# Kernel tuning notes

Measured on AMD Instinct MI355X. Metric: run time of the kernel, lower is better.

The kernel has to match this reference:

```python
import jax, jax.numpy as jnp
import numpy as np

N_NODES = 50000
N_EDGES = 800000
IN_DIM = 256
HID = 128
OUT = 128
HEADS = 2
EDGE_DIM = 2
NEG_SLOPE = 0.2


def _add_self_loops(src, dst, edge_attr, n):
    # PyG add_self_loops with fill_value='mean': self-loop edge_attr is the
    # mean of edge_attr over edges entering each node (0 if no in-edges).
    sums = jax.ops.segment_sum(edge_attr, dst, num_segments=n)
    cnt = jax.ops.segment_sum(jnp.ones((edge_attr.shape[0],), edge_attr.dtype), dst, num_segments=n)
    loop_attr = sums / jnp.maximum(cnt, 1.0)[:, None]
    ar = jnp.arange(n, dtype=src.dtype)
    return (jnp.concatenate([src, ar]), jnp.concatenate([dst, ar]),
            jnp.concatenate([edge_attr, loop_attr], axis=0))


def _gat_conv(x, src, dst, edge_attr, W, att_src, att_dst, We, att_e, bias, H, C):
    n = x.shape[0]
    xh = (x @ W).reshape(n, H, C)                      # [N,H,C]
    a_src = jnp.sum(xh * att_src, axis=-1)             # [N,H]
    a_dst = jnp.sum(xh * att_dst, axis=-1)             # [N,H]
    eh = (edge_attr @ We).reshape(-1, H, C)            # [E,H,C]
    a_e = jnp.sum(eh * att_e, axis=-1)                 # [E,H]
    logits = jax.nn.leaky_relu(a_src[src] + a_dst[dst] + a_e, NEG_SLOPE)
    # segment softmax over destination node
    m = jax.ops.segment_max(logits, dst, num_segments=n)
    m = jnp.where(jnp.isfinite(m), m, 0.0)
    ex = jnp.exp(logits - m[dst])
    denom = jax.ops.segment_sum(ex, dst, num_segments=n)
    alpha = ex / (denom[dst] + 1e-16)                  # [E,H]
    msg = xh[src] * alpha[:, :, None]                  # [E,H,C]
    out = jax.ops.segment_sum(msg, dst, num_segments=n)  # [N,H,C]
    return out.reshape(n, H * C) + bias


def setup_inputs() -> dict:
    key = jax.random.key(0)
    ks = jax.random.split(key, 16)
    s = 0.05
    inp = {
        "x": jax.random.normal(ks[0], (N_NODES, IN_DIM), jnp.float32),
        "edge_index": jax.random.randint(ks[1], (2, N_EDGES), 0, N_NODES, jnp.int32),
        "edge_attr": jax.random.normal(ks[2], (N_EDGES, EDGE_DIM), jnp.float32),
        # conv1: heads=2
        "W1": jax.random.normal(ks[3], (IN_DIM, HEADS * HID), jnp.float32) * s,
        "att_src1": jax.random.normal(ks[4], (HEADS, HID), jnp.float32) * s,
        "att_dst1": jax.random.normal(ks[5], (HEADS, HID), jnp.float32) * s,
        "We1": jax.random.normal(ks[6], (EDGE_DIM, HEADS * HID), jnp.float32) * s,
        "att_e1": jax.random.normal(ks[7], (HEADS, HID), jnp.float32) * s,
        "b1": jnp.zeros((HEADS * HID,), jnp.float32),
        # conv2: heads=1
        "W2": jax.random.normal(ks[8], (HEADS * HID, OUT), jnp.float32) * s,
        "att_src2": jax.random.normal(ks[9], (1, OUT), jnp.float32) * s,
        "att_dst2": jax.random.normal(ks[10], (1, OUT), jnp.float32) * s,
        "We2": jax.random.normal(ks[11], (EDGE_DIM, OUT), jnp.float32) * s,
        "att_e2": jax.random.normal(ks[12], (1, OUT), jnp.float32) * s,
        "b2": jnp.zeros((OUT,), jnp.float32),
    }
    return inp


def reference(x, edge_index, edge_attr, W1, att_src1, att_dst1, We1, att_e1, b1,
              W2, att_src2, att_dst2, We2, att_e2, b2):
    src, dst = edge_index[0], edge_index[1]
    src, dst, ea = _add_self_loops(src, dst, edge_attr, x.shape[0])
    h = _gat_conv(x, src, dst, ea, W1, att_src1, att_dst1, We1, att_e1, b1, HEADS, HID)
    h = jax.nn.elu(h)
    out = _gat_conv(h, src, dst, ea, W2, att_src2, att_dst2, We2, att_e2, b2, 1, OUT)
    return out
```

## Files before the change

### kernel.cpp

```cpp
#include <hip/hip_runtime.h>
#include <math.h>

#define N_NODES 50000
#define N_EDGES 800000
#define EP (N_EDGES + N_NODES)
#define NEG_SLOPE 0.2f
#define SCAN_BLOCKS ((N_NODES + 255) / 256)

typedef __attribute__((ext_vector_type(8))) short bf16x8;
typedef __attribute__((ext_vector_type(4))) float f32x4;

__device__ __forceinline__ unsigned short f2bf(float f) {
  unsigned u = __float_as_uint(f);
  unsigned r = (u + 0x7FFFu + ((u >> 16) & 1u)) >> 16;
  return (unsigned short)r;
}
__device__ __forceinline__ float bf2f(unsigned short b) {
  return __uint_as_float(((unsigned)b) << 16);
}

__global__ void fill_u32(unsigned* p, unsigned v, int n) {
  int i = blockIdx.x * blockDim.x + threadIdx.x;
  if (i < n) p[i] = v;
}

__global__ void rank_pass(const int* __restrict__ ei, int* __restrict__ cnt,
                          int* __restrict__ rank) {
  int e = blockIdx.x * blockDim.x + threadIdx.x;
  if (e >= N_EDGES) return;
  rank[e] = atomicAdd(&cnt[ei[N_EDGES + e]], 1);
}

__global__ void block_sums(const int* __restrict__ cnt, int* __restrict__ bsum) {
  __shared__ int ws[4];
  int b = blockIdx.x;
  int i = b * 256 + threadIdx.x;
  int v = (i < N_NODES) ? (cnt[i] + 1) : 0;
  #pragma unroll
  for (int off = 32; off > 0; off >>= 1) v += __shfl_down(v, off);
  if ((threadIdx.x & 63) == 0) ws[threadIdx.x >> 6] = v;
  __syncthreads();
  if (threadIdx.x == 0) bsum[b] = ws[0] + ws[1] + ws[2] + ws[3];
}

__global__ void emit_rowptr(const int* __restrict__ cnt, const int* __restrict__ bsum,
                            int* __restrict__ rowptr) {
  __shared__ int buf[2][256];
  int b = blockIdx.x, t = threadIdx.x;
  int vb = (t < SCAN_BLOCKS) ? bsum[t] : 0;
  buf[0][t] = vb;
  __syncthreads();
  int cur = 0;
  for (int off = 1; off < 256; off <<= 1) {
    int x = buf[cur][t];
    if (t >= off) x += buf[cur][t - off];
    buf[cur ^ 1][t] = x;
    cur ^= 1;
    __syncthreads();
  }
  int base = buf[cur][b] - ((b < SCAN_BLOCKS) ? bsum[b] : 0);
  __syncthreads();
  int i = b * 256 + t;
  int v = (i < N_NODES) ? (cnt[i] + 1) : 0;
  buf[cur][t] = v;
  __syncthreads();
  int c2 = cur;
  for (int off = 1; off < 256; off <<= 1) {
    int x = buf[c2][t];
    if (t >= off) x += buf[c2][t - off];
    buf[c2 ^ 1][t] = x;
    c2 ^= 1;
    __syncthreads();
  }
  int incl = buf[c2][t];
  if (i < N_NODES) {
    rowptr[i] = base + incl - v;
    if (i == N_NODES - 1) rowptr[N_NODES] = base + incl;
  }
}

__global__ void scatter_pass(const int* __restrict__ ei, const float* __restrict__ ea,
                             const int* __restrict__ rowptr, const int* __restrict__ rank,
                             uint2* __restrict__ ecsr) {
  int e = blockIdx.x * blockDim.x + threadIdx.x;
  if (e >= N_EDGES) return;
  int d = ei[N_EDGES + e];
  int pos = rowptr[d] + rank[e];
  uint2 v;
  v.x = (unsigned)ei[e];
  v.y = (unsigned)f2bf(ea[2 * e]) | ((unsigned)f2bf(ea[2 * e + 1]) << 16);
  ecsr[pos] = v;
}

#define MISC_LATTR 196
#define MISC_BT    384
__global__ void prep_misc(const int* __restrict__ rowptr, uint2* __restrict__ ecsr,
                          const float* __restrict__ W1, const float* __restrict__ W2,
                          unsigned short* __restrict__ b1h, unsigned short* __restrict__ b1l,
                          unsigned short* __restrict__ b2h, unsigned short* __restrict__ b2l,
                          const float* __restrict__ ae1, const float* __restrict__ ae2,
                          const float* __restrict__ We1, const float* __restrict__ We2,
                          float* __restrict__ Ae) {
  int b = blockIdx.x;
  int t = threadIdx.x;
  if (b < MISC_LATTR) {
    int n = b * 256 + t;
    if (n >= N_NODES) return;
    int beg = rowptr[n], end = rowptr[n + 1];
    float s0 = 0.f, s1 = 0.f;
    for (int j = beg; j < end - 1; ++j) {
      unsigned p = ecsr[j].y;
      s0 += __uint_as_float(p << 16);
      s1 += __uint_as_float(p & 0xFFFF0000u);
    }
    float c = fmaxf((float)(end - 1 - beg), 1.0f);
    uint2 m;
    m.x = (unsigned)n;
    m.y = (unsigned)f2bf(s0 / c) | ((unsigned)f2bf(s1 / c) << 16);
    ecsr[end - 1] = m;
  } else if (b < MISC_LATTR + MISC_BT) {
    int nb = b - MISC_LATTR;
    float v; unsigned short* ph; unsigned short* pl; int idx;
    if (nb < 256) { v = W1[t * 256 + nb];         ph = b1h; pl = b1l; idx = nb * 256 + t; }
    else          { v = W2[t * 128 + (nb - 256)]; ph = b2h; pl = b2l; idx = (nb - 256) * 256 + t; }
    unsigned short h = f2bf(v);
    ph[idx] = h;
    pl[idx] = f2bf(v - bf2f(h));
  } else {
    if (t >= 64) return;
    int bb = b - (MISC_LATTR + MISC_BT);
    float s = 0.f;
    if (bb < 4) {
      int d = bb >> 1, h = bb & 1;
      for (int c = t; c < 128; c += 64)
        s += We1[d * 256 + h * 128 + c] * ae1[h * 128 + c];
    } else {
      int d = bb - 4;
      for (int c = t; c < 128; c += 64)
        s += We2[d * 128 + c] * ae2[c];
    }
    for (int off = 32; off > 0; off >>= 1) s += __shfl_down(s, off);
    if (t == 0) Ae[bb] = s;
  }
}

template <int H>
__global__ __launch_bounds__(256) void gemm_split(
    const float* __restrict__ A,
    const unsigned short* __restrict__ Bth, const unsigned short* __restrict__ Btl,
    unsigned short* __restrict__ C, int M, int N,
    const float* __restrict__ att_src, const float* __restrict__ att_dst,
    float* __restrict__ asrc, float* __restrict__ adst) {
  __shared__ __attribute__((aligned(16))) unsigned short As[2][64][40];
  __shared__ __attribute__((aligned(16))) unsigned short Bs[2][128][40];
  __shared__ float redS[2][64], redD[2][64];
  int bm = blockIdx.y * 64, bn = blockIdx.x * 128;
  int tid = threadIdx.x;
  int l = tid & 63;
  int wid = tid >> 6;
  int wr = wid >> 1, wc = wid & 1;
  int rr = l & 15, kc = l >> 4;

  f32x4 acc[2][4];
  #pragma unroll
  for (int i = 0; i < 2; ++i)
    #pragma unroll
    for (int j = 0; j < 4; ++j)
      acc[i][j] = (f32x4){0.f, 0.f, 0.f, 0.f};

  int ar = tid >> 2, ac = tid & 3;
  int gm = bm + ar;

  for (int kt = 0; kt < 8; ++kt) {
    int k0 = kt * 32;
    float4 f0 = {0.f, 0.f, 0.f, 0.f}, f1 = f0;
    if (gm < M) {
      f0 = *(const float4*)(A + (size_t)gm * 256 + k0 + ac * 8);
      f1 = *(const float4*)(A + (size_t)gm * 256 + k0 + ac * 8 + 4);
    }
    float f[8] = {f0.x, f0.y, f0.z, f0.w, f1.x, f1.y, f1.z, f1.w};
    unsigned hw[4], lw[4];
    #pragma unroll
    for (int q = 0; q < 4; ++q) {
      unsigned short ha = f2bf(f[2 * q]),  hb = f2bf(f[2 * q + 1]);
      unsigned short la = f2bf(f[2 * q] - bf2f(ha)), lb = f2bf(f[2 * q + 1] - bf2f(hb));
      hw[q] = (unsigned)ha | ((unsigned)hb << 16);
      lw[q] = (unsigned)la | ((unsigned)lb << 16);
    }
    *(uint4*)&As[0][ar][ac * 8] = make_uint4(hw[0], hw[1], hw[2], hw[3]);
    *(uint4*)&As[1][ar][ac * 8] = make_uint4(lw[0], lw[1], lw[2], lw[3]);
    #pragma unroll
    for (int p = 0; p < 2; ++p) {
      int id = tid + p * 256;
      int nn = id >> 2, cc = id & 3;
      *(uint4*)&Bs[0][nn][cc * 8] = *(const uint4*)(Bth + (size_t)(bn + nn) * 256 + k0 + cc * 8);
      *(uint4*)&Bs[1][nn][cc * 8] = *(const uint4*)(Btl + (size_t)(bn + nn) * 256 + k0 + cc * 8);
    }
    __syncthreads();
    bf16x8 ah[2], alo[2], bh[4], bl[4];
    #pragma unroll
    for (int i = 0; i < 2; ++i) {
      ah[i]  = *(const bf16x8*)&As[0][wr * 32 + i * 16 + rr][kc * 8];
      alo[i] = *(const bf16x8*)&As[1][wr * 32 + i * 16 + rr][kc * 8];
    }
    #pragma unroll
    for (int j = 0; j < 4; ++j) {
      bh[j] = *(const bf16x8*)&Bs[0][wc * 64 + j * 16 + rr][kc * 8];
      bl[j] = *(const bf16x8*)&Bs[1][wc * 64 + j * 16 + rr][kc * 8];
    }
    #pragma unroll
    for (int i = 0; i < 2; ++i)
      #pragma unroll
      for (int j = 0; j < 4; ++j) {
        acc[i][j] = __builtin_amdgcn_mfma_f32_16x16x32_bf16(ah[i],  bh[j], acc[i][j], 0, 0, 0);
        acc[i][j] = __builtin_amdgcn_mfma_f32_16x16x32_bf16(ah[i],  bl[j], acc[i][j], 0, 0, 0);
        acc[i][j] = __builtin_amdgcn_mfma_f32_16x16x32_bf16(alo[i], bh[j], acc[i][j], 0, 0, 0);
      }
    __syncthreads();
  }

  #pragma unroll
  for (int i = 0; i < 2; ++i)
    #pragma unroll
    for (int reg = 0; reg < 4; ++reg) {
      int row = bm + wr * 32 + i * 16 + kc * 4 + reg;
      if (row < M) {
        #pragma unroll
        for (int j = 0; j < 4; ++j) {
          int col = bn + wc * 64 + j * 16 + rr;
          C[(size_t)row * N + col] = f2bf(acc[i][j][reg]);
        }
      }
    }

  int head = (H == 2) ? (bn >> 7) : 0;
  float ats[4], atd[4];
  #pragma unroll
  for (int j = 0; j < 4; ++j) {
    int colh = wc * 64 + j * 16 + rr;
    ats[j] = att_src[head * 128 + colh];
    atd[j] = att_dst[head * 128 + colh];
  }
  #pragma unroll
  for (int i = 0; i < 2; ++i)
    #pragma unroll
    for (int reg = 0; reg < 4; ++reg) {
      float sp = acc[i][0][reg] * ats[0] + acc[i][1][reg] * ats[1] +
                 acc[i][2][reg] * ats[2] + acc[i][3][reg] * ats[3];
      float dp = acc[i][0][reg] * atd[0] + acc[i][1][reg] * atd[1] +
                 acc[i][2][reg] * atd[2] + acc[i][3][reg] * atd[3];
      #pragma unroll
      for (int off = 1; off < 16; off <<= 1) {
        sp += __shfl_xor(sp, off);
        dp += __shfl_xor(dp, off);
      }
      if (rr == 0) {
        int row_local = wr * 32 + i * 16 + kc * 4 + reg;
        redS[wc][row_local] = sp;
        redD[wc][row_local] = dp;
      }
    }
  __syncthreads();
  if (tid < 64) {
    int row = bm + tid;
    if (row < M) {
      asrc[row * H + head] = redS[0][tid] + redS[1][tid];
      adst[row * H + head] = redD[0][tid] + redD[1][tid];
    }
  }
}

template <int H, int ACT>
__global__ __launch_bounds__(256)
void aggregate_fused(const unsigned short* __restrict__ xh, const float* __restrict__ asrc,
                     const float* __restrict__ adst, const uint2* __restrict__ ecsr,
                     const int* __restrict__ rowptr,
                     const float* __restrict__ Ae, int aeoff,
                     const float* __restrict__ bias, float* __restrict__ out) {
  constexpr int D = H * 128;
  constexpr int COLS = D / 64;
  __shared__ float exl[4][256][H];
  __shared__ int sl[4][256];
  int wid = threadIdx.x >> 6;
  int t = threadIdx.x & 63;
  int n = blockIdx.x * 4 + wid;
  if (n >= N_NODES) return;
  int beg = rowptr[n], end = rowptr[n + 1];
  int hA = t & (H - 1);
  float adnA = adst[n * H + hA];
  float Ae0 = Ae[aeoff + hA], Ae1 = Ae[aeoff + H + hA];
  int hB = (H == 2) ? (t >> 5) : 0;
  float lsum = 0.f;
  float acc[4][COLS];
  #pragma unroll
  for (int q = 0; q < 4; ++q)
    #pragma unroll
    for (int c = 0; c < COLS; ++c) acc[q][c] = 0.f;

  for (int cbeg = beg; cbeg < end; cbeg += 256) {
    int cnt = min(256, end - cbeg);
    for (int idx = t; idx < cnt * H; idx += 64) {
      int j0 = (H == 2) ? (idx >> 1) : idx;
      uint2 ev = ecsr[cbeg + j0];
      int s = (int)ev.x;
      float ea0 = __uint_as_float(ev.y << 16);
      float ea1 = __uint_as_float(ev.y & 0xFFFF0000u);
      float lg = asrc[s * H + hA] + adnA + ea0 * Ae0 + ea1 * Ae1;
      lg = (lg > 0.f) ? lg : NEG_SLOPE * lg;
      float ex = __expf(lg);
      exl[wid][j0][hA] = ex;
      if (hA == 0) sl[wid][j0] = s;
      lsum += ex;
    }
    asm volatile("s_waitcnt lgkmcnt(0)" ::: "memory");
    __builtin_amdgcn_sched_barrier(0);
    int j = 0;
    for (; j + 8 <= cnt; j += 8) {
      #pragma unroll
      for (int q = 0; q < 8; ++q) {
        float e = exl[wid][j + q][hB];
        int s = sl[wid][j + q];
        if (COLS == 4) {
          uint2 u = *(const uint2*)(xh + (size_t)s * D + 4 * t);
          acc[q & 3][0] = fmaf(e, __uint_as_float(u.x << 16), acc[q & 3][0]);
          acc[q & 3][1] = fmaf(e, __uint_as_float(u.x & 0xFFFF0000u), acc[q & 3][1]);
          acc[q & 3][2] = fmaf(e, __uint_as_float(u.y << 16), acc[q & 3][2]);
          acc[q & 3][3] = fmaf(e, __uint_as_float(u.y & 0xFFFF0000u), acc[q & 3][3]);
        } else {
          unsigned u = *(const unsigned*)(xh + (size_t)s * D + 2 * t);
          acc[q & 3][0] = fmaf(e, __uint_as_float(u << 16), acc[q & 3][0]);
          acc[q & 3][1] = fmaf(e, __uint_as_float(u & 0xFFFF0000u), acc[q & 3][1]);
        }
      }
    }
    for (; j < cnt; ++j) {
      float e = exl[wid][j][hB];
      int s = sl[wid][j];
      if (COLS == 4) {
        uint2 u = *(const uint2*)(xh + (size_t)s * D + 4 * t);
        acc[0][0] = fmaf(e, __uint_as_float(u.x << 16), acc[0][0]);
        acc[0][1] = fmaf(e, __uint_as_float(u.x & 0xFFFF0000u), acc[0][1]);
        acc[0][2] = fmaf(e, __uint_as_float(u.y << 16), acc[0][2]);
        acc[0][3] = fmaf(e, __uint_as_float(u.y & 0xFFFF0000u), acc[0][3]);
      } else {
        unsigned u = *(const unsigned*)(xh + (size_t)s * D + 2 * t);
        acc[0][0] = fmaf(e, __uint_as_float(u << 16), acc[0][0]);
        acc[0][1] = fmaf(e, __uint_as_float(u & 0xFFFF0000u), acc[0][1]);
      }
    }
    asm volatile("" ::: "memory");
  }

  #pragma unroll
  for (int off = H; off < 64; off <<= 1) lsum += __shfl_xor(lsum, off);
  float tot = (H == 2) ? __shfl(lsum, hB) : lsum;
  float inv = 1.0f / (tot + 1e-16f);

  float v[COLS];
  #pragma unroll
  for (int c = 0; c < COLS; ++c) {
    v[c] = fmaf(inv, (acc[0][c] + acc[1][c]) + (acc[2][c] + acc[3][c]),
                bias[COLS * t + c]);
    if (ACT) v[c] = (v[c] > 0.f) ? v[c] : expm1f(v[c]);
  }
  if (COLS == 4) {
    *(float4*)(out + (size_t)n * D + 4 * t) = make_float4(v[0], v[1], v[2], v[3]);
  } else {
    *(float2*)(out + (size_t)n * D + 2 * t) = make_float2(v[0], v[1]);
  }
}

extern "C" void kernel_launch(void* const* d_in, const int* in_sizes, int n_in,
                              void* d_out, int out_size, void* d_ws, size_t ws_size,
                              hipStream_t stream) {
  const float* x    = (const float*)d_in[0];
  const int*   ei   = (const int*)d_in[1];
  const float* ea   = (const float*)d_in[2];
  const float* W1   = (const float*)d_in[3];
  const float* as1  = (const float*)d_in[4];
  const float* ad1  = (const float*)d_in[5];
  const float* We1  = (const float*)d_in[6];
  const float* ae1  = (const float*)d_in[7];
  const float* b1   = (const float*)d_in[8];
  const float* W2   = (const float*)d_in[9];
  const float* as2  = (const float*)d_in[10];
  const float* ad2  = (const float*)d_in[11];
  const float* We2  = (const float*)d_in[12];
  const float* ae2  = (const float*)d_in[13];
  const float* b2   = (const float*)d_in[14];
  float* out = (float*)d_out;

  char* w = (char*)d_ws;
  size_t off = 0;
  auto alloc = [&](size_t bytes) -> void* {
    void* p = w + off;
    off = (off + bytes + 255) & ~(size_t)255;
    return p;
  };
  unsigned short* xhb   = (unsigned short*)alloc((size_t)N_NODES * 256 * 2);
  float*          hbuf  = (float*)alloc((size_t)N_NODES * 256 * 4);
  unsigned short* B1hi  = (unsigned short*)alloc(256 * 256 * 2);
  unsigned short* B1lo  = (unsigned short*)alloc(256 * 256 * 2);
  unsigned short* B2hi  = (unsigned short*)alloc(128 * 256 * 2);
  unsigned short* B2lo  = (unsigned short*)alloc(128 * 256 * 2);
  int*      rowptr   = (int*)alloc((N_NODES + 1) * 4);
  int*      cnt      = (int*)alloc(N_NODES * 4);
  int*      rank     = (int*)alloc((size_t)N_EDGES * 4);
  int*      bsum     = (int*)alloc(256 * 4);
  uint2*    ecsr     = (uint2*)alloc((size_t)EP * 8);
  float*    asrc     = (float*)alloc(N_NODES * 2 * 4);
  float*    adst     = (float*)alloc(N_NODES * 2 * 4);
  float*    Ae       = (float*)alloc(16 * 4);

  auto cdiv = [](int a, int b) { return (a + b - 1) / b; };

  fill_u32<<<cdiv(N_NODES, 256), 256, 0, stream>>>((unsigned*)cnt, 0u, N_NODES);
  rank_pass<<<cdiv(N_EDGES, 256), 256, 0, stream>>>(ei, cnt, rank);
  block_sums<<<SCAN_BLOCKS, 256, 0, stream>>>(cnt, bsum);
  emit_rowptr<<<SCAN_BLOCKS, 256, 0, stream>>>(cnt, bsum, rowptr);
  scatter_pass<<<cdiv(N_EDGES, 256), 256, 0, stream>>>(ei, ea, rowptr, rank, ecsr);
  prep_misc<<<MISC_LATTR + MISC_BT + 6, 256, 0, stream>>>(rowptr, ecsr, W1, W2,
                                                          B1hi, B1lo, B2hi, B2lo,
                                                          ae1, ae2, We1, We2, Ae);

  gemm_split<2><<<dim3(2, cdiv(N_NODES, 64)), 256, 0, stream>>>(x, B1hi, B1lo, xhb, N_NODES, 256,
                                                                as1, ad1, asrc, adst);
  aggregate_fused<2, 1><<<cdiv(N_NODES, 4), 256, 0, stream>>>(xhb, asrc, adst, ecsr, rowptr,
                                                              Ae, 0, b1, hbuf);

  gemm_split<1><<<dim3(1, cdiv(N_NODES, 64)), 256, 0, stream>>>(hbuf, B2hi, B2lo, xhb, N_NODES, 128,
                                                                as2, ad2, asrc, adst);
  aggregate_fused<1, 0><<<cdiv(N_NODES, 4), 256, 0, stream>>>(xhb, asrc, adst, ecsr, rowptr,
                                                              Ae, 4, b2, out);
}
```

Baseline: 248.0 us.

## Privatize in-degree counters into eight copies and use one-wave aggregation blocks

Edge ranking now uses eight private counter arrays, chosen by block index, so that concurrent atomics on the same destination node contend less. A new combine kernel turns these into per-copy offsets and total counts, and the scatter pass adds the per-copy offset. The aggregation kernels now launch one 64-thread block per node instead of four nodes per 256-thread block, which stops short-degree waves from holding a block's shared memory while they wait. This adds an extra kernel, extra counter memory traffic, and far more small blocks to schedule.

```diff
diff --git a/kernel.cpp b/kernel.cpp
--- a/kernel.cpp
+++ b/kernel.cpp
@@ -24,11 +24,25 @@
   if (i < n) p[i] = v;
 }
 
-__global__ void rank_pass(const int* __restrict__ ei, int* __restrict__ cnt,
-                          int* __restrict__ rank) {
+__global__ void rank_pass8(const int* __restrict__ ei, int* __restrict__ cnt8,
+                           int* __restrict__ rank) {
   int e = blockIdx.x * blockDim.x + threadIdx.x;
   if (e >= N_EDGES) return;
-  rank[e] = atomicAdd(&cnt[ei[N_EDGES + e]], 1);
+  int c = blockIdx.x & 7;
+  rank[e] = atomicAdd(&cnt8[c * N_NODES + ei[N_EDGES + e]], 1);
+}
+
+__global__ void combine8(int* __restrict__ cnt8, int* __restrict__ cnt) {
+  int n = blockIdx.x * blockDim.x + threadIdx.x;
+  if (n >= N_NODES) return;
+  int running = 0;
+  #pragma unroll
+  for (int c = 0; c < 8; ++c) {
+    int v = cnt8[c * N_NODES + n];
+    cnt8[c * N_NODES + n] = running;
+    running += v;
+  }
+  cnt[n] = running;
 }
 
 __global__ void block_sums(const int* __restrict__ cnt, int* __restrict__ bsum) {
@@ -81,11 +95,12 @@
 
 __global__ void scatter_pass(const int* __restrict__ ei, const float* __restrict__ ea,
                              const int* __restrict__ rowptr, const int* __restrict__ rank,
-                             uint2* __restrict__ ecsr) {
+                             const int* __restrict__ cnt8, uint2* __restrict__ ecsr) {
   int e = blockIdx.x * blockDim.x + threadIdx.x;
   if (e >= N_EDGES) return;
   int d = ei[N_EDGES + e];
-  int pos = rowptr[d] + rank[e];
+  int c = blockIdx.x & 7;
+  int pos = rowptr[d] + cnt8[c * N_NODES + d] + rank[e];
   uint2 v;
   v.x = (unsigned)ei[e];
   v.y = (unsigned)f2bf(ea[2 * e]) | ((unsigned)f2bf(ea[2 * e + 1]) << 16);
@@ -271,7 +286,7 @@
 }
 
 template <int H, int ACT>
-__global__ __launch_bounds__(256)
+__global__ __launch_bounds__(64)
 void aggregate_fused(const unsigned short* __restrict__ xh, const float* __restrict__ asrc,
                      const float* __restrict__ adst, const uint2* __restrict__ ecsr,
                      const int* __restrict__ rowptr,
@@ -279,12 +294,10 @@
                      const float* __restrict__ bias, float* __restrict__ out) {
   constexpr int D = H * 128;
   constexpr int COLS = D / 64;
-  __shared__ float exl[4][256][H];
-  __shared__ int sl[4][256];
-  int wid = threadIdx.x >> 6;
-  int t = threadIdx.x & 63;
-  int n = blockIdx.x * 4 + wid;
-  if (n >= N_NODES) return;
+  __shared__ float exl[256][H];
+  __shared__ int sl[256];
+  int n = blockIdx.x;
+  int t = threadIdx.x;
   int beg = rowptr[n], end = rowptr[n + 1];
   int hA = t & (H - 1);
   float adnA = adst[n * H + hA];
@@ -308,18 +321,17 @@
       float lg = asrc[s * H + hA] + adnA + ea0 * Ae0 + ea1 * Ae1;
       lg = (lg > 0.f) ? lg : NEG_SLOPE * lg;
       float ex = __expf(lg);
-      exl[wid][j0][hA] = ex;
-      if (hA == 0) sl[wid][j0] = s;
+      exl[j0][hA] = ex;
+      if (hA == 0) sl[j0] = s;
       lsum += ex;
     }
-    asm volatile("s_waitcnt lgkmcnt(0)" ::: "memory");
-    __builtin_amdgcn_sched_barrier(0);
+    __syncthreads();
     int j = 0;
     for (; j + 8 <= cnt; j += 8) {
       #pragma unroll
       for (int q = 0; q < 8; ++q) {
-        float e = exl[wid][j + q][hB];
-        int s = sl[wid][j + q];
+        float e = exl[j + q][hB];
+        int s = sl[j + q];
         if (COLS == 4) {
           uint2 u = *(const uint2*)(xh + (size_t)s * D + 4 * t);
           acc[q & 3][0] = fmaf(e, __uint_as_float(u.x << 16), acc[q & 3][0]);
@@ -334,8 +346,8 @@
       }
     }
     for (; j < cnt; ++j) {
-      float e = exl[wid][j][hB];
-      int s = sl[wid][j];
+      float e = exl[j][hB];
+      int s = sl[j];
       if (COLS == 4) {
         uint2 u = *(const uint2*)(xh + (size_t)s * D + 4 * t);
         acc[0][0] = fmaf(e, __uint_as_float(u.x << 16), acc[0][0]);
@@ -348,7 +360,7 @@
         acc[0][1] = fmaf(e, __uint_as_float(u & 0xFFFF0000u), acc[0][1]);
       }
     }
-    asm volatile("" ::: "memory");
+    __syncthreads();
   }
 
   #pragma unroll
@@ -405,6 +417,7 @@
   unsigned short* B2lo  = (unsigned short*)alloc(128 * 256 * 2);
   int*      rowptr   = (int*)alloc((N_NODES + 1) * 4);
   int*      cnt      = (int*)alloc(N_NODES * 4);
+  int*      cnt8     = (int*)alloc((size_t)N_NODES * 8 * 4);
   int*      rank     = (int*)alloc((size_t)N_EDGES * 4);
   int*      bsum     = (int*)alloc(256 * 4);
   uint2*    ecsr     = (uint2*)alloc((size_t)EP * 8);
@@ -414,22 +427,23 @@
 
   auto cdiv = [](int a, int b) { return (a + b - 1) / b; };
 
-  fill_u32<<<cdiv(N_NODES, 256), 256, 0, stream>>>((unsigned*)cnt, 0u, N_NODES);
-  rank_pass<<<cdiv(N_EDGES, 256), 256, 0, stream>>>(ei, cnt, rank);
+  fill_u32<<<cdiv(N_NODES * 8, 256), 256, 0, stream>>>((unsigned*)cnt8, 0u, N_NODES * 8);
+  rank_pass8<<<cdiv(N_EDGES, 256), 256, 0, stream>>>(ei, cnt8, rank);
+  combine8<<<cdiv(N_NODES, 256), 256, 0, stream>>>(cnt8, cnt);
   block_sums<<<SCAN_BLOCKS, 256, 0, stream>>>(cnt, bsum);
   emit_rowptr<<<SCAN_BLOCKS, 256, 0, stream>>>(cnt, bsum, rowptr);
-  scatter_pass<<<cdiv(N_EDGES, 256), 256, 0, stream>>>(ei, ea, rowptr, rank, ecsr);
+  scatter_pass<<<cdiv(N_EDGES, 256), 256, 0, stream>>>(ei, ea, rowptr, rank, cnt8, ecsr);
   prep_misc<<<MISC_LATTR + MISC_BT + 6, 256, 0, stream>>>(rowptr, ecsr, W1, W2,
                                                           B1hi, B1lo, B2hi, B2lo,
                                                           ae1, ae2, We1, We2, Ae);
 
   gemm_split<2><<<dim3(2, cdiv(N_NODES, 64)), 256, 0, stream>>>(x, B1hi, B1lo, xhb, N_NODES, 256,
                                                                 as1, ad1, asrc, adst);
-  aggregate_fused<2, 1><<<cdiv(N_NODES, 4), 256, 0, stream>>>(xhb, asrc, adst, ecsr, rowptr,
-                                                              Ae, 0, b1, hbuf);
+  aggregate_fused<2, 1><<<N_NODES, 64, 0, stream>>>(xhb, asrc, adst, ecsr, rowptr,
+                                                    Ae, 0, b1, hbuf);
 
   gemm_split<1><<<dim3(1, cdiv(N_NODES, 64)), 256, 0, stream>>>(hbuf, B2hi, B2lo, xhb, N_NODES, 128,
                                                                 as2, ad2, asrc, adst);
-  aggregate_fused<1, 0><<<cdiv(N_NODES, 4), 256, 0, stream>>>(xhb, asrc, adst, ecsr, rowptr,
-                                                              Ae, 4, b2, out);
-}
+  aggregate_fused<1, 0><<<N_NODES, 64, 0, stream>>>(xhb, asrc, adst, ecsr, rowptr,
+                                                    Ae, 4, b2, out);
+}
```

New measurement: 237.2 us. 1.05x faster.
